# Performance work log

Hardware: AMD Instinct MI355X
Metric: run time of the kernel (lower is better)

## Reference

```python
import jax, jax.numpy as jnp
import numpy as np

# GlobalAttention block from GATESynergy: to_dense_batch -> multi-head
# masked self-attention per graph -> scatter back to sparse + residual.
B, NMAX, DIN, DOUT, H = 512, 160, 128, 128, 4
DH = DOUT // H  # 32
COUNTS = np.where(np.arange(B) % 2 == 0, 96, 160)  # nodes per graph, sum=65536
T = int(COUNTS.sum())


def _xavier(key, dout, din):
    lim = np.sqrt(6.0 / (din + dout)).astype(np.float32)
    return jax.random.uniform(key, (dout, din), jnp.float32, -lim, lim)


def setup_inputs() -> dict:
    key = jax.random.key(0)
    ks = jax.random.split(key, 5)
    batch = jnp.asarray(np.repeat(np.arange(B), COUNTS), dtype=jnp.int32)
    x = jax.random.normal(ks[0], (T, DIN), jnp.float32)
    return {
        "x": x,
        "batch": batch,
        "Wq": _xavier(ks[1], DOUT, DIN), "bq": jnp.zeros((DOUT,), jnp.float32),
        "Wk": _xavier(ks[2], DOUT, DIN), "bk": jnp.zeros((DOUT,), jnp.float32),
        "Wv": _xavier(ks[3], DOUT, DIN), "bv": jnp.zeros((DOUT,), jnp.float32),
        "Wo": _xavier(ks[4], DOUT, DOUT), "bo": jnp.zeros((DOUT,), jnp.float32),
    }


def reference(x, batch, Wq, bq, Wk, bk, Wv, bv, Wo, bo):
    n = x.shape[0]
    # --- to_dense_batch: sparse [T, D] -> dense [B, NMAX, D] + mask ---
    counts = jax.ops.segment_sum(jnp.ones(n, jnp.int32), batch, num_segments=B)
    starts = jnp.cumsum(counts) - counts            # first node index per graph
    pos = jnp.arange(n, dtype=jnp.int32) - starts[batch]  # slot within graph
    x_dense = jnp.zeros((B, NMAX, DIN), x.dtype).at[batch, pos].set(x)
    mask = jnp.zeros((B, NMAX), bool).at[batch, pos].set(True)

    def proj(W, b):  # [B,N,DIN] -> [B,H,N,DH]
        return (x_dense @ W.T + b).reshape(B, NMAX, H, DH).transpose(0, 2, 1, 3)

    q, k, v = proj(Wq, bq), proj(Wk, bk), proj(Wv, bv)
    scores = jnp.einsum('bhnd,bhmd->bhnm', q, k) / jnp.sqrt(jnp.asarray(DH, x.dtype))
    scores = jnp.where(mask[:, None, None, :], scores, -jnp.inf)  # mask keys
    attn = jax.nn.softmax(scores, axis=-1)  # dropout p=0.0 -> identity
    out = jnp.einsum('bhnm,bhmd->bnhd', attn, v).reshape(B, NMAX, DOUT)
    out = out @ Wo.T + bo
    out_sparse = out[batch, pos]  # gather valid nodes back to sparse layout
    return out_sparse + x  # residual: in_channels == out_channels
```

## Files before the change

### kernel.cpp

```cpp
#include <hip/hip_runtime.h>

typedef unsigned short u16;
typedef unsigned int u32;
typedef __attribute__((ext_vector_type(8))) short bf16x8;
typedef __attribute__((ext_vector_type(4))) float f32x4;

__device__ __forceinline__ u16 f2bf(float f) {
  u32 u = __builtin_bit_cast(u32, f);
  u += 0x7fffu + ((u >> 16) & 1u);
  return (u16)(u >> 16);
}
__device__ __forceinline__ short f2bs(float f) { return (short)f2bf(f); }

__device__ __forceinline__ bf16x8 cvt8(const float* p) {
  f32x4 a = *reinterpret_cast<const f32x4*>(p);
  f32x4 b = *reinterpret_cast<const f32x4*>(p + 4);
  bf16x8 r;
  r[0] = f2bs(a[0]); r[1] = f2bs(a[1]); r[2] = f2bs(a[2]); r[3] = f2bs(a[3]);
  r[4] = f2bs(b[0]); r[5] = f2bs(b[1]); r[6] = f2bs(b[2]); r[7] = f2bs(b[3]);
  return r;
}
__device__ __forceinline__ bf16x8 lds8(const u16* p) {
  return *reinterpret_cast<const bf16x8*>(p);
}

#define MFMA(a, b, c) __builtin_amdgcn_mfma_f32_16x16x32_bf16((a), (b), (c), 0, 0, 0)

constexpr int DIN = 128, DOUT = 128, DH = 32;
constexpr int T = 65536;
constexpr size_t WFOFF = 0;
constexpr size_t QOFF = 65536;
constexpr size_t KOFF = QOFF + (size_t)4 * T * DH;
constexpr size_t VOFF = KOFF + (size_t)4 * T * DH;
constexpr size_t WS_NEED = (VOFF + (size_t)4 * T * DH) * 2;

__device__ __forceinline__ size_t fragoff(int mat, int ft, int ks) {
  return ((size_t)((mat * 8 + ft) * 4 + ks)) << 9;
}

__global__ void cvtw_kernel(const float* __restrict__ Wq, const float* __restrict__ Wk,
                            const float* __restrict__ Wv, const float* __restrict__ Wo,
                            u16* __restrict__ wf) {
  const int fl = blockIdx.x * 256 + threadIdx.x;
  const int lane = fl & 63, ks = (fl >> 6) & 3, ft = (fl >> 8) & 7, mat = fl >> 11;
  const float* src = mat == 0 ? Wq : mat == 1 ? Wk : mat == 2 ? Wv : Wo;
  const int lr = lane & 15, lg = lane >> 4;
  bf16x8 r = cvt8(src + (ft * 16 + lr) * DIN + ks * 32 + lg * 8);
  *reinterpret_cast<bf16x8*>(wf + (size_t)fl * 8) = r;
}

__global__ __launch_bounds__(256, 3) void qkv_kernel(const float* __restrict__ x,
                                                     const float* __restrict__ bq,
                                                     const float* __restrict__ bk,
                                                     const float* __restrict__ bv,
                                                     u16* __restrict__ ws) {
  const int tid = threadIdx.x;
  const int w = tid >> 6, lane = tid & 63, lg = lane >> 4, lr = lane & 15;
  const size_t rbase = (size_t)blockIdx.x * 128 + w * 32;
  const f32x4 zero = {0.f, 0.f, 0.f, 0.f};
  const u16* wf = ws + WFOFF;
  u16* Q = ws + QOFF;
  u16* K = ws + KOFF;
  u16* V = ws + VOFF;

  bf16x8 xa[2][4];
#pragma unroll
  for (int rt = 0; rt < 2; ++rt)
#pragma unroll
    for (int ks = 0; ks < 4; ++ks)
      xa[rt][ks] = cvt8(x + (rbase + rt * 16 + lr) * DIN + ks * 32 + lg * 8);

#pragma unroll
  for (int ft = 0; ft < 8; ++ft) {
    const int h = ft >> 1, dt = ft & 1;
    bf16x8 wqf[4], wkf[4], wvf[4];
#pragma unroll
    for (int ks = 0; ks < 4; ++ks) {
      wqf[ks] = lds8(wf + fragoff(0, ft, ks) + lane * 8);
      wkf[ks] = lds8(wf + fragoff(1, ft, ks) + lane * 8);
      wvf[ks] = lds8(wf + fragoff(2, ft, ks) + lane * 8);
    }
    f32x4 qacc[2], kacc[2], vacc[2];
#pragma unroll
    for (int rt = 0; rt < 2; ++rt) qacc[rt] = kacc[rt] = vacc[rt] = zero;
#pragma unroll
    for (int rt = 0; rt < 2; ++rt)
#pragma unroll
      for (int ks = 0; ks < 4; ++ks) {
        qacc[rt] = MFMA(xa[rt][ks], wqf[ks], qacc[rt]);
        kacc[rt] = MFMA(xa[rt][ks], wkf[ks], kacc[rt]);
        vacc[rt] = MFMA(wvf[ks], xa[rt][ks], vacc[rt]);
      }
    const float bqv = bq[ft * 16 + lr], bkv = bk[ft * 16 + lr];
    float bvj[4];
#pragma unroll
    for (int j = 0; j < 4; ++j) bvj[j] = bv[ft * 16 + lg * 4 + j];
#pragma unroll
    for (int rt = 0; rt < 2; ++rt) {
      const size_t row0 = rbase + rt * 16;
      const size_t qk_base = (size_t)h * T * DH + (row0 + lg * 4) * DH + dt * 16 + lr;
      const size_t v_base = (size_t)h * T * DH + (((rbase >> 5) + (rt >> 1)) << 10) +
                            (size_t)(dt * 16 + lg * 4) * 32 + (rt & 1) * 16 + lr;
#pragma unroll
      for (int j = 0; j < 4; ++j) {
        Q[qk_base + (size_t)j * DH] = f2bf(qacc[rt][j] + bqv);
        K[qk_base + (size_t)j * DH] = f2bf(kacc[rt][j] + bkv);
        V[v_base + (size_t)j * 32] = f2bf(vacc[rt][j] + bvj[j]);
      }
    }
  }
}

template <int C>
__device__ void attn_wave2(const u16* __restrict__ Qh, const u16* __restrict__ Kh,
                           const u16* __restrict__ Vh, const u16* __restrict__ wf,
                           const float* __restrict__ bo, const float* __restrict__ x,
                           float* __restrict__ out, int start, int h, int t0,
                           u16 (&strip)[16][168], u16 (&otile)[2][16][136]) {
  constexpr int NT = C / 16, KB = C / 32;
  const int lane = threadIdx.x & 63, lg = lane >> 4, lr = lane & 15;
  const f32x4 zero = {0.f, 0.f, 0.f, 0.f};
  const int w = h;

  bf16x8 vb[KB][2];
#pragma unroll
  for (int ks = 0; ks < KB; ++ks)
#pragma unroll
    for (int dt = 0; dt < 2; ++dt)
      vb[ks][dt] = lds8(Vh + (((size_t)(start >> 5) + ks) << 10) +
                        (size_t)(dt * 16 + lr) * 32 + lg * 8);
  bf16x8 kf[NT];
#pragma unroll
  for (int ct = 0; ct < NT; ++ct)
    kf[ct] = lds8(Kh + (size_t)(start + ct * 16 + lr) * DH + lg * 8);

#pragma unroll
  for (int r = 0; r < 2; ++r) {
    const int gr = start + (t0 + r) * 16;
    const bf16x8 qa = lds8(Qh + (size_t)(gr + lr) * DH + lg * 8);
    f32x4 sacc[NT];
#pragma unroll
    for (int ct = 0; ct < NT; ++ct) sacc[ct] = MFMA(qa, kf[ct], zero);

    const float scale = 0.17677669529663687f;
    float s[4];
#pragma unroll
    for (int j = 0; j < 4; ++j) {
      s[j] = 0.f;
#pragma unroll
      for (int ct = 0; ct < NT; ++ct) {
        const float p = __expf(sacc[ct][j] * scale);
        sacc[ct][j] = p;
        s[j] += p;
      }
    }
#pragma unroll
    for (int d = 1; d < 16; d <<= 1) {
#pragma unroll
      for (int j = 0; j < 4; ++j) s[j] += __shfl_xor(s[j], d, 64);
    }
#pragma unroll
    for (int j = 0; j < 4; ++j) {
      const float inv = 1.0f / s[j];
#pragma unroll
      for (int ct = 0; ct < NT; ++ct)
        strip[lg * 4 + j][ct * 16 + lr] = f2bf(sacc[ct][j] * inv);
    }
    asm volatile("s_waitcnt lgkmcnt(0)" ::: "memory");

    f32x4 o0 = zero, o1 = zero;
#pragma unroll
    for (int ks = 0; ks < KB; ++ks) {
      const bf16x8 pa = lds8(&strip[lr][ks * 32 + lg * 8]);
      o0 = MFMA(pa, vb[ks][0], o0);
      o1 = MFMA(pa, vb[ks][1], o1);
    }
#pragma unroll
    for (int j = 0; j < 4; ++j) {
      otile[r][lg * 4 + j][h * 32 + lr] = f2bf(o0[j]);
      otile[r][lg * 4 + j][h * 32 + 16 + lr] = f2bf(o1[j]);
    }
  }

  const int c0 = w * 32 + lr, c1 = w * 32 + 16 + lr;
  float xr0[2][4], xr1[2][4];
#pragma unroll
  for (int r = 0; r < 2; ++r) {
    const int gr = start + (t0 + r) * 16;
#pragma unroll
    for (int j = 0; j < 4; ++j) {
      const size_t n = (size_t)gr + lg * 4 + j;
      xr0[r][j] = x[n * DIN + c0];
      xr1[r][j] = x[n * DIN + c1];
    }
  }
  __syncthreads();

  const float b0 = bo[c0], b1 = bo[c1];
#pragma unroll
  for (int r = 0; r < 2; ++r) {
    bf16x8 oa[4];
#pragma unroll
    for (int ks = 0; ks < 4; ++ks) oa[ks] = lds8(&otile[r][lr][ks * 32 + lg * 8]);
    f32x4 acc0 = zero, acc1 = zero;
#pragma unroll
    for (int ks = 0; ks < 4; ++ks) {
      acc0 = MFMA(oa[ks], lds8(wf + fragoff(3, w * 2, ks) + lane * 8), acc0);
      acc1 = MFMA(oa[ks], lds8(wf + fragoff(3, w * 2 + 1, ks) + lane * 8), acc1);
    }
    const int gr = start + (t0 + r) * 16;
#pragma unroll
    for (int j = 0; j < 4; ++j) {
      const size_t n = (size_t)gr + lg * 4 + j;
      out[n * DOUT + c0] = acc0[j] + b0 + xr0[r][j];
      out[n * DOUT + c1] = acc1[j] + b1 + xr1[r][j];
    }
  }
}

__global__ __launch_bounds__(256, 3) void attn_kernel(const u16* __restrict__ ws,
                                                      const float* __restrict__ bo,
                                                      const float* __restrict__ x,
                                                      float* __restrict__ out) {
  __shared__ u16 strip[4][16][168];
  __shared__ u16 otile[2][16][136];
  const int w = threadIdx.x >> 6;
  const int phys = blockIdx.x;
  const int xcd = phys & 7, idx = phys >> 3;
  const int u = idx & 7;
  const int p = (idx >> 3) * 8 + xcd;
  const int h = w;
  const int t0 = u * 2;
  const u16* Qh = ws + QOFF + (size_t)h * T * DH;
  const u16* Kh = ws + KOFF + (size_t)h * T * DH;
  const u16* Vh = ws + VOFF + (size_t)h * T * DH;
  const u16* wf = ws + WFOFF;

  if (t0 < 6)
    attn_wave2<96>(Qh, Kh, Vh, wf, bo, x, out, p * 256, h, t0, strip[w], otile);
  else
    attn_wave2<160>(Qh, Kh, Vh, wf, bo, x, out, p * 256 + 96, h, t0 - 6, strip[w], otile);
}

struct SLds1 {
  u16 k[160][40];
  u16 vt[32][168];
  u16 strip[4][16][168];
};

template <int C>
__device__ void attn1(const float* __restrict__ xg, const float* __restrict__ Wq,
                      const float* __restrict__ bq, const float* __restrict__ Wk,
                      const float* __restrict__ bk, const float* __restrict__ Wv,
                      const float* __restrict__ bv, float* __restrict__ og, int h, SLds1& sm) {
  constexpr int NT = C / 16, KB = C / 32, SLOTS = (NT + 3) / 4;
  const int tid = threadIdx.x;
  const int w = tid >> 6, lane = tid & 63, lg = lane >> 4, lr = lane & 15;
  const f32x4 zero = {0.f, 0.f, 0.f, 0.f};

  for (int t = w; t < 2 * NT; t += 4) {
    const int rt = t >> 1, dt = t & 1;
    f32x4 kacc = zero, vacc = zero;
#pragma unroll
    for (int ks = 0; ks < 4; ++ks) {
      bf16x8 xa = cvt8(xg + (rt * 16 + lr) * DIN + ks * 32 + lg * 8);
      bf16x8 wk = cvt8(Wk + (h * DH + dt * 16 + lr) * DIN + ks * 32 + lg * 8);
      bf16x8 wv = cvt8(Wv + (h * DH + dt * 16 + lr) * DIN + ks * 32 + lg * 8);
      kacc = MFMA(xa, wk, kacc);
      vacc = MFMA(wv, xa, vacc);
    }
    const float kb_ = bk[h * DH + dt * 16 + lr];
#pragma unroll
    for (int j = 0; j < 4; ++j) {
      sm.k[rt * 16 + lg * 4 + j][dt * 16 + lr] = f2bf(kacc[j] + kb_);
      sm.vt[dt * 16 + lg * 4 + j][rt * 16 + lr] = f2bf(vacc[j] + bv[h * DH + dt * 16 + lg * 4 + j]);
    }
  }
  __syncthreads();

#pragma unroll
  for (int sl = 0; sl < SLOTS; ++sl) {
    const int rt = w + sl * 4;
    if (rt < NT) {
#pragma unroll
      for (int dt = 0; dt < 2; ++dt) {
        f32x4 qacc = zero;
#pragma unroll
        for (int ks = 0; ks < 4; ++ks) {
          bf16x8 xa = cvt8(xg + (rt * 16 + lr) * DIN + ks * 32 + lg * 8);
          bf16x8 wq = cvt8(Wq + (h * DH + dt * 16 + lr) * DIN + ks * 32 + lg * 8);
          qacc = MFMA(xa, wq, qacc);
        }
        const float bias = bq[h * DH + dt * 16 + lr];
#pragma unroll
        for (int j = 0; j < 4; ++j)
          sm.strip[w][lg * 4 + j][dt * 16 + lr] = f2bf(qacc[j] + bias);
      }
      asm volatile("s_waitcnt lgkmcnt(0)" ::: "memory");
      const bf16x8 qa = lds8(&sm.strip[w][lr][lg * 8]);
      f32x4 sacc[NT];
#pragma unroll
      for (int ct = 0; ct < NT; ++ct)
        sacc[ct] = MFMA(qa, lds8(&sm.k[ct * 16 + lr][lg * 8]), zero);
      const float scale = 0.17677669529663687f;
      float m[4], s[4];
#pragma unroll
      for (int j = 0; j < 4; ++j) {
        m[j] = sacc[0][j];
#pragma unroll
        for (int ct = 1; ct < NT; ++ct) m[j] = fmaxf(m[j], sacc[ct][j]);
      }
#pragma unroll
      for (int d = 1; d < 16; d <<= 1)
#pragma unroll
        for (int j = 0; j < 4; ++j) m[j] = fmaxf(m[j], __shfl_xor(m[j], d, 64));
#pragma unroll
      for (int j = 0; j < 4; ++j) {
        s[j] = 0.f;
#pragma unroll
        for (int ct = 0; ct < NT; ++ct) {
          const float p = __expf((sacc[ct][j] - m[j]) * scale);
          sacc[ct][j] = p;
          s[j] += p;
        }
      }
#pragma unroll
      for (int d = 1; d < 16; d <<= 1)
#pragma unroll
        for (int j = 0; j < 4; ++j) s[j] += __shfl_xor(s[j], d, 64);
#pragma unroll
      for (int j = 0; j < 4; ++j) {
        const float inv = 1.0f / s[j];
#pragma unroll
        for (int ct = 0; ct < NT; ++ct)
          sm.strip[w][lg * 4 + j][ct * 16 + lr] = f2bf(sacc[ct][j] * inv);
      }
      asm volatile("s_waitcnt lgkmcnt(0)" ::: "memory");
      f32x4 o0 = zero, o1 = zero;
#pragma unroll
      for (int ks = 0; ks < KB; ++ks) {
        const bf16x8 pa = lds8(&sm.strip[w][lr][ks * 32 + lg * 8]);
        o0 = MFMA(pa, lds8(&sm.vt[lr][ks * 32 + lg * 8]), o0);
        o1 = MFMA(pa, lds8(&sm.vt[16 + lr][ks * 32 + lg * 8]), o1);
      }
#pragma unroll
      for (int j = 0; j < 4; ++j) {
        const int n = rt * 16 + lg * 4 + j;
        og[n * DOUT + h * DH + lr] = o0[j];
        og[n * DOUT + h * DH + 16 + lr] = o1[j];
      }
    }
  }
}

__global__ __launch_bounds__(256, 3) void fb_k1(const float* __restrict__ x,
                                                const float* __restrict__ Wq,
                                                const float* __restrict__ bq,
                                                const float* __restrict__ Wk,
                                                const float* __restrict__ bk,
                                                const float* __restrict__ Wv,
                                                const float* __restrict__ bv,
                                                float* __restrict__ O) {
  __shared__ SLds1 sm;
  const int bid = blockIdx.x;
  const int g = bid >> 2, h = bid & 3;
  const int p = g >> 1;
  if (g & 1)
    attn1<160>(x + (size_t)(p * 256 + 96) * DIN, Wq, bq, Wk, bk, Wv, bv,
               O + (size_t)(p * 256 + 96) * DOUT, h, sm);
  else
    attn1<96>(x + (size_t)(p * 256) * DIN, Wq, bq, Wk, bk, Wv, bv, O + (size_t)(p * 256) * DOUT,
              h, sm);
}

__global__ __launch_bounds__(256, 4) void fb_k2(float* __restrict__ io, const float* __restrict__ x,
                                                const float* __restrict__ Wo,
                                                const float* __restrict__ bo) {
  const int tid = threadIdx.x;
  const int w = tid >> 6, lane = tid & 63, lg = lane >> 4, lr = lane & 15;
  const f32x4 zero = {0.f, 0.f, 0.f, 0.f};
  const int rbase = blockIdx.x * 128 + w * 32;
  bf16x8 oa[2][4];
#pragma unroll
  for (int r = 0; r < 2; ++r)
#pragma unroll
    for (int ks = 0; ks < 4; ++ks)
      oa[r][ks] = cvt8(io + (size_t)(rbase + r * 16 + lr) * DOUT + ks * 32 + lg * 8);
  f32x4 acc[2][8];
#pragma unroll
  for (int r = 0; r < 2; ++r)
#pragma unroll
    for (int jt = 0; jt < 8; ++jt) acc[r][jt] = zero;
#pragma unroll
  for (int jt = 0; jt < 8; ++jt)
#pragma unroll
    for (int ks = 0; ks < 4; ++ks) {
      const bf16x8 wb = cvt8(Wo + (size_t)(jt * 16 + lr) * DOUT + ks * 32 + lg * 8);
      acc[0][jt] = MFMA(oa[0][ks], wb, acc[0][jt]);
      acc[1][jt] = MFMA(oa[1][ks], wb, acc[1][jt]);
    }
#pragma unroll
  for (int r = 0; r < 2; ++r)
#pragma unroll
    for (int jt = 0; jt < 8; ++jt) {
      const int c = jt * 16 + lr;
      const float bias = bo[c];
#pragma unroll
      for (int j = 0; j < 4; ++j) {
        const size_t n = (size_t)rbase + r * 16 + lg * 4 + j;
        io[n * DOUT + c] = acc[r][jt][j] + bias + x[n * DIN + c];
      }
    }
}

extern "C" void kernel_launch(void* const* d_in, const int* in_sizes, int n_in,
                              void* d_out, int out_size, void* d_ws, size_t ws_size,
                              hipStream_t stream) {
  const float* x = (const float*)d_in[0];
  const float* Wq = (const float*)d_in[2];
  const float* bq = (const float*)d_in[3];
  const float* Wk = (const float*)d_in[4];
  const float* bk = (const float*)d_in[5];
  const float* Wv = (const float*)d_in[6];
  const float* bv = (const float*)d_in[7];
  const float* Wo = (const float*)d_in[8];
  const float* bo = (const float*)d_in[9];
  float* out = (float*)d_out;

  if (ws_size >= WS_NEED) {
    u16* ws = (u16*)d_ws;
    cvtw_kernel<<<dim3(32), dim3(256), 0, stream>>>(Wq, Wk, Wv, Wo, ws);
    qkv_kernel<<<dim3(512), dim3(256), 0, stream>>>(x, bq, bk, bv, ws);
    attn_kernel<<<dim3(2048), dim3(256), 0, stream>>>(ws, bo, x, out);
  } else {
    fb_k1<<<dim3(2048), dim3(256), 0, stream>>>(x, Wq, bq, Wk, bk, Wv, bv, out);
    fb_k2<<<dim3(512), dim3(256), 0, stream>>>(out, x, Wo, bo);
  }
}
```

Before: 56.15 us.

## Process half a graph per block to amortize K/V fragment loads

Each attention block now handles 3 or 5 query row tiles of one graph instead of 2, so the grid shrinks from 2048 to 1024 blocks. The K and V fragments each wave loads are reused across more query tiles, cutting redundant global loads. The residual x prefetch before the barrier is removed and x is now read inline at the output store. In exchange the output tile buffer in shared memory grows, 160-node blocks carry more work than 96-node blocks, and there are fewer blocks to hide latency.

```diff
diff --git a/kernel.cpp b/kernel.cpp
--- a/kernel.cpp
+++ b/kernel.cpp
@@ -111,12 +111,12 @@
   }
 }
 
-template <int C>
-__device__ void attn_wave2(const u16* __restrict__ Qh, const u16* __restrict__ Kh,
+template <int C, int NTILES>
+__device__ void attn_waveQ(const u16* __restrict__ Qh, const u16* __restrict__ Kh,
                            const u16* __restrict__ Vh, const u16* __restrict__ wf,
                            const float* __restrict__ bo, const float* __restrict__ x,
                            float* __restrict__ out, int start, int h, int t0,
-                           u16 (&strip)[16][168], u16 (&otile)[2][16][136]) {
+                           u16 (&strip)[16][168], u16 (&otile)[5][16][136]) {
   constexpr int NT = C / 16, KB = C / 32;
   const int lane = threadIdx.x & 63, lg = lane >> 4, lr = lane & 15;
   const f32x4 zero = {0.f, 0.f, 0.f, 0.f};
@@ -135,7 +135,7 @@
     kf[ct] = lds8(Kh + (size_t)(start + ct * 16 + lr) * DH + lg * 8);
 
 #pragma unroll
-  for (int r = 0; r < 2; ++r) {
+  for (int r = 0; r < NTILES; ++r) {
     const int gr = start + (t0 + r) * 16;
     const bf16x8 qa = lds8(Qh + (size_t)(gr + lr) * DH + lg * 8);
     f32x4 sacc[NT];
@@ -181,24 +181,12 @@
       otile[r][lg * 4 + j][h * 32 + 16 + lr] = f2bf(o1[j]);
     }
   }
+  __syncthreads();
 
   const int c0 = w * 32 + lr, c1 = w * 32 + 16 + lr;
-  float xr0[2][4], xr1[2][4];
-#pragma unroll
-  for (int r = 0; r < 2; ++r) {
-    const int gr = start + (t0 + r) * 16;
-#pragma unroll
-    for (int j = 0; j < 4; ++j) {
-      const size_t n = (size_t)gr + lg * 4 + j;
-      xr0[r][j] = x[n * DIN + c0];
-      xr1[r][j] = x[n * DIN + c1];
-    }
-  }
-  __syncthreads();
-
   const float b0 = bo[c0], b1 = bo[c1];
 #pragma unroll
-  for (int r = 0; r < 2; ++r) {
+  for (int r = 0; r < NTILES; ++r) {
     bf16x8 oa[4];
 #pragma unroll
     for (int ks = 0; ks < 4; ++ks) oa[ks] = lds8(&otile[r][lr][ks * 32 + lg * 8]);
@@ -212,8 +200,8 @@
 #pragma unroll
     for (int j = 0; j < 4; ++j) {
       const size_t n = (size_t)gr + lg * 4 + j;
-      out[n * DOUT + c0] = acc0[j] + b0 + xr0[r][j];
-      out[n * DOUT + c1] = acc1[j] + b1 + xr1[r][j];
+      out[n * DOUT + c0] = acc0[j] + b0 + x[n * DIN + c0];
+      out[n * DOUT + c1] = acc1[j] + b1 + x[n * DIN + c1];
     }
   }
 }
@@ -223,23 +211,25 @@
                                                       const float* __restrict__ x,
                                                       float* __restrict__ out) {
   __shared__ u16 strip[4][16][168];
-  __shared__ u16 otile[2][16][136];
+  __shared__ u16 otile[5][16][136];
   const int w = threadIdx.x >> 6;
   const int phys = blockIdx.x;
   const int xcd = phys & 7, idx = phys >> 3;
-  const int u = idx & 7;
-  const int p = (idx >> 3) * 8 + xcd;
-  const int h = w;
-  const int t0 = u * 2;
-  const u16* Qh = ws + QOFF + (size_t)h * T * DH;
-  const u16* Kh = ws + KOFF + (size_t)h * T * DH;
-  const u16* Vh = ws + VOFF + (size_t)h * T * DH;
+  const int q = idx & 3;
+  const int p = (idx >> 2) * 8 + xcd;
+  const u16* Qh = ws + QOFF + (size_t)w * T * DH;
+  const u16* Kh = ws + KOFF + (size_t)w * T * DH;
+  const u16* Vh = ws + VOFF + (size_t)w * T * DH;
   const u16* wf = ws + WFOFF;
 
-  if (t0 < 6)
-    attn_wave2<96>(Qh, Kh, Vh, wf, bo, x, out, p * 256, h, t0, strip[w], otile);
+  if (q == 0)
+    attn_waveQ<96, 3>(Qh, Kh, Vh, wf, bo, x, out, p * 256, w, 0, strip[w], otile);
+  else if (q == 1)
+    attn_waveQ<96, 3>(Qh, Kh, Vh, wf, bo, x, out, p * 256, w, 3, strip[w], otile);
+  else if (q == 2)
+    attn_waveQ<160, 5>(Qh, Kh, Vh, wf, bo, x, out, p * 256 + 96, w, 0, strip[w], otile);
   else
-    attn_wave2<160>(Qh, Kh, Vh, wf, bo, x, out, p * 256 + 96, h, t0 - 6, strip[w], otile);
+    attn_waveQ<160, 5>(Qh, Kh, Vh, wf, bo, x, out, p * 256 + 96, w, 5, strip[w], otile);
 }
 
 struct SLds1 {
@@ -431,7 +421,7 @@
     u16* ws = (u16*)d_ws;
     cvtw_kernel<<<dim3(32), dim3(256), 0, stream>>>(Wq, Wk, Wv, Wo, ws);
     qkv_kernel<<<dim3(512), dim3(256), 0, stream>>>(x, bq, bk, bv, ws);
-    attn_kernel<<<dim3(2048), dim3(256), 0, stream>>>(ws, bo, x, out);
+    attn_kernel<<<dim3(1024), dim3(256), 0, stream>>>(ws, bo, x, out);
   } else {
     fb_k1<<<dim3(2048), dim3(256), 0, stream>>>(x, Wq, bq, Wk, bk, Wv, bv, out);
     fb_k2<<<dim3(512), dim3(256), 0, stream>>>(out, x, Wo, bo);
```

After: 70.65 us. +25.8%, slower.
